# Performance work log

Measured on AMD Instinct MI355X. Metric: run time of the kernel, lower is better.

The kernel has to match this reference:

```python
import jax, jax.numpy as jnp
from jax import lax
import numpy as np

B_SZ, L, NH, DH, DS = 2, 2048, 24, 64, 128


def setup_inputs() -> dict:
    key = jax.random.key(0)
    k1, k2, k3, k4 = jax.random.split(key, 4)
    x = jax.random.normal(k1, (B_SZ, L, NH, DH), dtype=jnp.float32)
    A = jax.random.normal(k2, (B_SZ, L, NH), dtype=jnp.float32)
    B_mat = jax.random.normal(k3, (B_SZ, L, NH, DS), dtype=jnp.float32)
    C_mat = jax.random.normal(k4, (B_SZ, L, NH, DS), dtype=jnp.float32)
    delta_param = jnp.zeros((NH,), dtype=jnp.float32)
    return {"x": x, "A": A, "B_mat": B_mat, "C_mat": C_mat, "delta_param": delta_param}


def reference(x, A, B_mat, C_mat, delta_param):
    # x: (B, L, nh, dh); A: (B, L, nh); B_mat/C_mat: (B, L, nh, ds)
    b, l, nh, dh = x.shape
    ds = B_mat.shape[-1]
    delta = jax.nn.softplus(A + delta_param[None, None, :])        # (B, L, nh)
    A_bar = jnp.exp(-delta * jnp.abs(A))                            # (B, L, nh)

    def step(h, inp):
        x_t, B_t, C_t, a_t = inp  # (B,nh,dh), (B,nh,ds), (B,nh,ds), (B,nh)
        h = a_t[:, :, None, None] * h + x_t[..., None] * B_t[:, :, None, :]
        y_t = jnp.einsum('bhds,bhs->bhd', h, C_t)                   # (B, nh, dh)
        return h, y_t

    h0 = jnp.zeros((b, nh, dh, ds), dtype=x.dtype)
    xs = (jnp.moveaxis(x, 1, 0),      # (L, B, nh, dh)
          jnp.moveaxis(B_mat, 1, 0),  # (L, B, nh, ds)
          jnp.moveaxis(C_mat, 1, 0),  # (L, B, nh, ds)
          jnp.moveaxis(A_bar, 1, 0))  # (L, B, nh)
    _, ys = lax.scan(step, h0, xs)    # ys: (L, B, nh, dh)
    return jnp.moveaxis(ys, 0, 1)     # (B, L, nh, dh)
```

## Files before the change

kernel.cpp:

```cpp
#include <hip/hip_runtime.h>

#define B_SZ 2
#define LSEQ 2048
#define NHh 24
#define DHh 64
#define DSs 128
#define TCH 64
#define NC  (LSEQ / TCH)
#define BH  (B_SZ * NHh)

#define S_ELEMS   (BH * LSEQ)
#define G_ELEMS   ((size_t)BH * NC * DSs * DHh)
#define WS_S_BYTES ((size_t)S_ELEMS * 4)
#define WS_G_BYTES (G_ELEMS * 2)
#define WS_REQ     (WS_S_BYTES + 2 * WS_G_BYTES)

#define SP  136
#define UP  72

typedef __attribute__((ext_vector_type(8))) short bf16x8;
typedef __attribute__((ext_vector_type(4))) float f32x4;

__device__ __forceinline__ unsigned short f2bf(float f) {
    union { float f; unsigned u; } v; v.f = f;
    unsigned r = ((v.u >> 16) & 1u) + 0x7FFFu;
    return (unsigned short)((v.u + r) >> 16);
}
__device__ __forceinline__ float bf2f(unsigned short h) {
    union { unsigned u; float f; } v; v.u = ((unsigned)h) << 16; return v.f;
}
__device__ __forceinline__ unsigned pk2(float a, float b) {
    return (unsigned)f2bf(a) | ((unsigned)f2bf(b) << 16);
}

__global__ __launch_bounds__(256, 2)
void k1_chunk(const float* __restrict__ x, const float* __restrict__ A,
              const float* __restrict__ Bm, const float* __restrict__ dp,
              float* __restrict__ S_ws, unsigned short* __restrict__ G_ws) {
    __shared__ __align__(16) unsigned short sBT[DSs][UP];
    __shared__ __align__(16) unsigned short sXT[DHh][UP];
    __shared__ float sF[TCH];

    const int c  = blockIdx.x & (NC - 1);
    const int bh = blockIdx.x >> 5;
    const int nh = bh % NHh; const int b = bh / NHh;
    const int tid = threadIdx.x;
    const int lane = tid & 63;
    const int w = tid >> 6;

    const size_t row0 = (size_t)(b * LSEQ + c * TCH) * NHh + nh;

    const int u = tid >> 2;
    const int q = tid & 3;
    const float* Brow = Bm + (row0 + (size_t)u * NHh) * DSs;
    const float* xrow = x  + (row0 + (size_t)u * NHh) * DHh;
    float4 bv[8], xv[4];
    #pragma unroll
    for (int j = 0; j < 8; ++j) bv[j] = *(const float4*)(Brow + (j * 4 + q) * 4);
    #pragma unroll
    for (int j = 0; j < 4; ++j) xv[j] = *(const float4*)(xrow + (j * 4 + q) * 4);

    if (tid < 64) {
        float a  = A[row0 + (size_t)tid * NHh];
        float z  = a + dp[nh];
        float sp = (z > 20.0f) ? z : log1pf(expf(z));
        float la = -sp * fabsf(a);
        #pragma unroll
        for (int off = 1; off < 64; off <<= 1) {
            float v = __shfl_up(la, off, 64);
            if (lane >= off) la += v;
        }
        S_ws[(size_t)bh * LSEQ + c * TCH + tid] = la;
        float s63 = __shfl(la, 63, 64);
        sF[tid] = expf(s63 - la);
    }
    __syncthreads();

    #pragma unroll
    for (int j = 0; j < 8; ++j) {
        const int s = (j * 4 + q) * 4;
        sBT[s + 0][u] = f2bf(bv[j].x);
        sBT[s + 1][u] = f2bf(bv[j].y);
        sBT[s + 2][u] = f2bf(bv[j].z);
        sBT[s + 3][u] = f2bf(bv[j].w);
    }
    const float f = sF[u];
    #pragma unroll
    for (int j = 0; j < 4; ++j) {
        const int d = (j * 4 + q) * 4;
        sXT[d + 0][u] = f2bf(xv[j].x * f);
        sXT[d + 1][u] = f2bf(xv[j].y * f);
        sXT[d + 2][u] = f2bf(xv[j].z * f);
        sXT[d + 3][u] = f2bf(xv[j].w * f);
    }
    __syncthreads();

    const int fr = lane >> 4, fc = lane & 15;
    bf16x8 afr0 = *(const bf16x8*)&sXT[16 * w + fc][fr * 8];
    bf16x8 afr1 = *(const bf16x8*)&sXT[16 * w + fc][32 + fr * 8];
    #pragma unroll
    for (int st = 0; st < 8; ++st) {
        f32x4 acc = {0.f, 0.f, 0.f, 0.f};
        bf16x8 b0 = *(const bf16x8*)&sBT[st * 16 + fc][fr * 8];
        bf16x8 b1 = *(const bf16x8*)&sBT[st * 16 + fc][32 + fr * 8];
        acc = __builtin_amdgcn_mfma_f32_16x16x32_bf16(afr0, b0, acc, 0, 0, 0);
        acc = __builtin_amdgcn_mfma_f32_16x16x32_bf16(afr1, b1, acc, 0, 0, 0);
        unsigned short* gout = G_ws +
            ((((size_t)bh * NC + c) * DHh + 16 * w + fr * 4) * DSs) + st * 16 + fc;
        #pragma unroll
        for (int r = 0; r < 4; ++r) gout[(size_t)r * DSs] = f2bf(acc[r]);
    }
}

__global__ __launch_bounds__(256)
void k2_scan(const float* __restrict__ S_ws, const unsigned short* __restrict__ G_ws,
             unsigned short* __restrict__ H_ws) {
    const int dblk = blockIdx.x & 3;
    const int bh   = blockIdx.x >> 2;
    const int tid  = threadIdx.x;
    const int d    = dblk * 16 + (tid >> 4);
    const int s0   = (tid & 15) * 8;

    float h[8];
    #pragma unroll
    for (int k = 0; k < 8; ++k) h[k] = 0.f;

    size_t base = (((size_t)bh * NC) * DHh + d) * DSs + s0;
    const size_t cstride = (size_t)DHh * DSs;

    uint4 gv = *(const uint4*)(G_ws + base);
    for (int c = 0; c < NC; ++c) {
        uint4 gn = (c + 1 < NC) ? *(const uint4*)(G_ws + base + (size_t)(c + 1) * cstride) : gv;
        const float e = expf(S_ws[(size_t)bh * LSEQ + c * TCH + (TCH - 1)]);
        uint4 p;
        p.x = pk2(h[0], h[1]); p.y = pk2(h[2], h[3]);
        p.z = pk2(h[4], h[5]); p.w = pk2(h[6], h[7]);
        *(uint4*)(H_ws + base + (size_t)c * cstride) = p;
        const unsigned gu[4] = {gv.x, gv.y, gv.z, gv.w};
        #pragma unroll
        for (int k = 0; k < 4; ++k) {
            h[2 * k]     = fmaf(e, h[2 * k],     bf2f((unsigned short)(gu[k] & 0xffff)));
            h[2 * k + 1] = fmaf(e, h[2 * k + 1], bf2f((unsigned short)(gu[k] >> 16)));
        }
        gv = gn;
    }
}

__global__ __launch_bounds__(256, 2)
void k3_y(const float* __restrict__ x, const float* __restrict__ Bm,
          const float* __restrict__ Cm, const float* __restrict__ S_ws,
          const unsigned short* __restrict__ H_ws, float* __restrict__ y) {
    __shared__ __align__(16) unsigned short sC[TCH][SP];
    __shared__ __align__(16) unsigned short sB[TCH][SP];
    __shared__ __align__(16) unsigned short sH[DHh][SP];
    __shared__ __align__(16) unsigned short sW[TCH][UP];
    __shared__ __align__(16) unsigned short sXT[DHh][UP];
    __shared__ float sS[TCH];
    __shared__ float sEt[TCH];

    const int c  = blockIdx.x & (NC - 1);
    const int bh = blockIdx.x >> 5;
    const int nh = bh % NHh; const int b = bh / NHh;
    const int tid = threadIdx.x;
    const int lane = tid & 63;
    const int w = tid >> 6;

    const size_t row0 = (size_t)(b * LSEQ + c * TCH) * NHh + nh;

    const int rr = tid >> 2;
    const int q  = tid & 3;
    const float* Crow = Cm + (row0 + (size_t)rr * NHh) * DSs;
    const float* Brow = Bm + (row0 + (size_t)rr * NHh) * DSs;
    const float* xrow = x  + (row0 + (size_t)rr * NHh) * DHh;
    const unsigned short* Hrow = H_ws + (((size_t)bh * NC + c) * DHh + rr) * DSs;
    float4 cv[8], bv[8], xv[4];
    uint4  hv[4];
    #pragma unroll
    for (int j = 0; j < 8; ++j) cv[j] = *(const float4*)(Crow + (j * 4 + q) * 4);
    #pragma unroll
    for (int j = 0; j < 8; ++j) bv[j] = *(const float4*)(Brow + (j * 4 + q) * 4);
    #pragma unroll
    for (int j = 0; j < 4; ++j) xv[j] = *(const float4*)(xrow + (j * 4 + q) * 4);
    #pragma unroll
    for (int j = 0; j < 4; ++j) hv[j] = *(const uint4*)(Hrow + (j * 4 + q) * 8);

    if (tid < 64) {
        float sv = S_ws[(size_t)bh * LSEQ + c * TCH + tid];
        sS[tid]  = sv;
        sEt[tid] = expf(sv);
    }

    #pragma unroll
    for (int j = 0; j < 8; ++j) {
        const int s = (j * 4 + q) * 4;
        *(uint2*)&sC[rr][s] = make_uint2(pk2(cv[j].x, cv[j].y), pk2(cv[j].z, cv[j].w));
        *(uint2*)&sB[rr][s] = make_uint2(pk2(bv[j].x, bv[j].y), pk2(bv[j].z, bv[j].w));
    }
    #pragma unroll
    for (int j = 0; j < 4; ++j)
        *(uint4*)&sH[rr][(j * 4 + q) * 8] = hv[j];
    #pragma unroll
    for (int j = 0; j < 4; ++j) {
        const int d = (j * 4 + q) * 4;
        sXT[d + 0][rr] = f2bf(xv[j].x);
        sXT[d + 1][rr] = f2bf(xv[j].y);
        sXT[d + 2][rr] = f2bf(xv[j].z);
        sXT[d + 3][rr] = f2bf(xv[j].w);
    }
    __syncthreads();

    const int fr = lane >> 4, fc = lane & 15;
    const int t0w = 16 * w;

    bf16x8 ca[4];
    #pragma unroll
    for (int kb = 0; kb < 4; ++kb)
        ca[kb] = *(const bf16x8*)&sC[t0w + fc][kb * 32 + fr * 8];
    float st4[4];
    #pragma unroll
    for (int r = 0; r < 4; ++r) st4[r] = sS[t0w + fr * 4 + r];

    #pragma unroll
    for (int ut = 0; ut < 4; ++ut) {
        const int u0 = ut * 16;
        unsigned short wv[4] = {0, 0, 0, 0};
        if (ut <= w) {
            f32x4 acc = {0.f, 0.f, 0.f, 0.f};
            #pragma unroll
            for (int kb = 0; kb < 4; ++kb) {
                bf16x8 bb = *(const bf16x8*)&sB[u0 + fc][kb * 32 + fr * 8];
                acc = __builtin_amdgcn_mfma_f32_16x16x32_bf16(ca[kb], bb, acc, 0, 0, 0);
            }
            const float su = sS[u0 + fc];
            const int   uu = u0 + fc;
            #pragma unroll
            for (int r = 0; r < 4; ++r) {
                const int t = t0w + fr * 4 + r;
                const float dd = fminf(st4[r] - su, 0.f);
                const float val = (uu <= t) ? acc[r] * expf(dd) : 0.f;
                wv[r] = f2bf(val);
            }
        }
        #pragma unroll
        for (int r = 0; r < 4; ++r) sW[t0w + fr * 4 + r][u0 + fc] = wv[r];
    }

    bf16x8 wa0 = *(const bf16x8*)&sW[t0w + fc][fr * 8];
    bf16x8 wa1;
    if (w >= 2) wa1 = *(const bf16x8*)&sW[t0w + fc][32 + fr * 8];
    float et4[4];
    #pragma unroll
    for (int r = 0; r < 4; ++r) et4[r] = sEt[t0w + fr * 4 + r];

    #pragma unroll
    for (int dt = 0; dt < 4; ++dt) {
        const int d0 = dt * 16;
        f32x4 acc = {0.f, 0.f, 0.f, 0.f};
        #pragma unroll
        for (int kb = 0; kb < 4; ++kb) {
            bf16x8 hb = *(const bf16x8*)&sH[d0 + fc][kb * 32 + fr * 8];
            acc = __builtin_amdgcn_mfma_f32_16x16x32_bf16(ca[kb], hb, acc, 0, 0, 0);
        }
        #pragma unroll
        for (int r = 0; r < 4; ++r) acc[r] *= et4[r];
        bf16x8 xb0 = *(const bf16x8*)&sXT[d0 + fc][fr * 8];
        acc = __builtin_amdgcn_mfma_f32_16x16x32_bf16(wa0, xb0, acc, 0, 0, 0);
        if (w >= 2) {
            bf16x8 xb1 = *(const bf16x8*)&sXT[d0 + fc][32 + fr * 8];
            acc = __builtin_amdgcn_mfma_f32_16x16x32_bf16(wa1, xb1, acc, 0, 0, 0);
        }
        float* yout = y + (row0 + (size_t)(t0w + fr * 4) * NHh) * DHh + d0 + fc;
        #pragma unroll
        for (int r = 0; r < 4; ++r) yout[(size_t)r * NHh * DHh] = acc[r];
    }
}

__device__ __forceinline__ void gload_lds16(const float* g, void* l) {
    __builtin_amdgcn_global_load_lds(
        (const __attribute__((address_space(1))) void*)g,
        (__attribute__((address_space(3))) void*)l, 16, 0, 0);
}
__device__ __forceinline__ void gload_lds4(const float* g, float* l) {
    __builtin_amdgcn_global_load_lds(
        (const __attribute__((address_space(1))) void*)g,
        (__attribute__((address_space(3))) void*)l, 4, 0, 0);
}
#define F_DBLK 4
#define F_DPW 16
#define F_TCH 32
#define F_NCH (LSEQ / F_TCH)
__global__ __launch_bounds__(256, 1)
void ssm_scan_fb(const float* __restrict__ x, const float* __restrict__ A,
                 const float* __restrict__ Bm, const float* __restrict__ Cm,
                 const float* __restrict__ dp, float* __restrict__ y) {
    __shared__ float s_abar[LSEQ];
    __shared__ float s_B[2][F_TCH][DSs];
    __shared__ float s_C[2][F_TCH][DSs];
    __shared__ float s_x[2][F_TCH][F_DPW];
    const int blk = blockIdx.x;
    const int dblk = blk % F_DBLK, bh = blk / F_DBLK;
    const int nh = bh % NHh, b = bh / NHh;
    const float dpv = dp[nh];
    for (int i = threadIdx.x; i < LSEQ; i += 256) {
        float a = A[(b * LSEQ + i) * NHh + nh];
        float z = a + dpv;
        float sp = (z > 20.0f) ? z : log1pf(expf(z));
        s_abar[i] = expf(-sp * fabsf(a));
    }
    const int tid = threadIdx.x, wid = tid >> 6, lane = tid & 63;
    const int dloc = tid >> 4, sg = tid & 15, sb = sg * 8;
    const size_t bh_off = (size_t)(b * LSEQ) * NHh + nh;
    const float* Bbase = Bm + bh_off * DSs;
    const float* Cbase = Cm + bh_off * DSs;
    const float* xbase = x + bh_off * DHh + dblk * F_DPW;
    float* yp = y + bh_off * DHh + dblk * F_DPW + dloc;
    const int RSTRIDE = NHh * DSs, XSTRIDE = NHh * DHh;
    auto stage = [&](int buf, int t0) {
        #pragma unroll
        for (int j = 0; j < 4; ++j) {
            const int r0 = (wid * 4 + j) * 2, r = r0 + (lane >> 5), col = (lane & 31) * 4;
            gload_lds16(Bbase + (size_t)(t0 + r) * RSTRIDE + col, &s_B[buf][r0][0]);
            gload_lds16(Cbase + (size_t)(t0 + r) * RSTRIDE + col, &s_C[buf][r0][0]);
        }
        #pragma unroll
        for (int j = 0; j < 2; ++j) {
            const int idx = (wid * 2 + j) * 64 + lane, t = idx >> 4, dc = idx & 15;
            gload_lds4(xbase + (size_t)(t0 + t) * XSTRIDE + dc, &s_x[buf][(wid * 2 + j) * 4][0]);
        }
    };
    stage(0, 0);
    __syncthreads();
    float h0=0,h1=0,h2=0,h3=0,h4=0,h5=0,h6=0,h7=0;
    for (int c = 0; c < F_NCH; ++c) {
        const int buf = c & 1;
        if (c + 1 < F_NCH) stage(buf ^ 1, (c + 1) * F_TCH);
        const int t0 = c * F_TCH;
        #pragma unroll 4
        for (int tt = 0; tt < F_TCH; ++tt) {
            const int t = t0 + tt;
            const float a = s_abar[t], xd = s_x[buf][tt][dloc];
            const float4* Br = (const float4*)&s_B[buf][tt][sb];
            const float4* Cr = (const float4*)&s_C[buf][tt][sb];
            const float4 B0 = Br[0], B1 = Br[1], C0 = Cr[0], C1 = Cr[1];
            h0 = fmaf(a, h0, xd * B0.x); h1 = fmaf(a, h1, xd * B0.y);
            h2 = fmaf(a, h2, xd * B0.z); h3 = fmaf(a, h3, xd * B0.w);
            h4 = fmaf(a, h4, xd * B1.x); h5 = fmaf(a, h5, xd * B1.y);
            h6 = fmaf(a, h6, xd * B1.z); h7 = fmaf(a, h7, xd * B1.w);
            float p0 = h0 * C0.x; p0 = fmaf(h1, C0.y, p0); p0 = fmaf(h2, C0.z, p0); p0 = fmaf(h3, C0.w, p0);
            float p1 = h4 * C1.x; p1 = fmaf(h5, C1.y, p1); p1 = fmaf(h6, C1.z, p1); p1 = fmaf(h7, C1.w, p1);
            float p = p0 + p1;
            p += __shfl_xor(p, 1, 64); p += __shfl_xor(p, 2, 64);
            p += __shfl_xor(p, 4, 64); p += __shfl_xor(p, 8, 64);
            if (sg == 0) yp[(size_t)t * XSTRIDE] = p;
        }
        __syncthreads();
    }
}

extern "C" void kernel_launch(void* const* d_in, const int* in_sizes, int n_in,
                              void* d_out, int out_size, void* d_ws, size_t ws_size,
                              hipStream_t stream) {
    const float* x  = (const float*)d_in[0];
    const float* A  = (const float*)d_in[1];
    const float* Bm = (const float*)d_in[2];
    const float* Cm = (const float*)d_in[3];
    const float* dp = (const float*)d_in[4];
    float* y = (float*)d_out;

    if (ws_size >= WS_REQ) {
        float* S_ws = (float*)d_ws;
        unsigned short* G_ws = (unsigned short*)((char*)d_ws + WS_S_BYTES);
        unsigned short* H_ws = G_ws + G_ELEMS;
        hipLaunchKernelGGL(k1_chunk, dim3(BH * NC), dim3(256), 0, stream,
                           x, A, Bm, dp, S_ws, G_ws);
        hipLaunchKernelGGL(k2_scan, dim3(BH * 4), dim3(256), 0, stream,
                           S_ws, G_ws, H_ws);
        hipLaunchKernelGGL(k3_y, dim3(BH * NC), dim3(256), 0, stream,
                           x, Bm, Cm, S_ws, H_ws, y);
    } else {
        hipLaunchKernelGGL(ssm_scan_fb, dim3(BH * F_DBLK), dim3(256), 0, stream,
                           x, A, Bm, Cm, dp, y);
    }
}
```

Baseline: 188.9 us.

## Precompute bf16 swizzled B/C/x planes in k1 and DMA them into k3 LDS

k1 now also reads C and writes bf16 copies of B, C and raw x into workspace, laid out as XOR-swizzled planes. k3 then loads these planes straight into LDS with global_load_lds instead of loading fp32 rows and converting them through registers. k2 writes H in the same swizzled layout, caches the per-chunk decay exponentials in LDS and prefetches G two chunks ahead. This cuts k3's fp32 read traffic and conversion work but adds extra bf16 workspace writes in k1 and raises workspace size. If the workspace is too small, the fallback kernel runs instead.

```diff
diff --git a/kernel.cpp b/kernel.cpp
--- a/kernel.cpp
+++ b/kernel.cpp
@@ -9,14 +9,15 @@
 #define NC  (LSEQ / TCH)
 #define BH  (B_SZ * NHh)
 
-#define S_ELEMS   (BH * LSEQ)
-#define G_ELEMS   ((size_t)BH * NC * DSs * DHh)
-#define WS_S_BYTES ((size_t)S_ELEMS * 4)
-#define WS_G_BYTES (G_ELEMS * 2)
-#define WS_REQ     (WS_S_BYTES + 2 * WS_G_BYTES)
-
-#define SP  136
 #define UP  72
+
+#define S_ELEMS    ((size_t)BH * LSEQ)
+#define PLANE128   ((size_t)TCH * DSs)
+#define PLANE64    ((size_t)TCH * DHh)
+#define P128_ELEMS ((size_t)BH * NC * PLANE128)
+#define P64_ELEMS  ((size_t)BH * NC * PLANE64)
+#define WS_S_BYTES (S_ELEMS * 4)
+#define WS_REQ     (WS_S_BYTES + 4 * P128_ELEMS * 2 + P64_ELEMS * 2)
 
 typedef __attribute__((ext_vector_type(8))) short bf16x8;
 typedef __attribute__((ext_vector_type(4))) float f32x4;
@@ -32,13 +33,21 @@
 __device__ __forceinline__ unsigned pk2(float a, float b) {
     return (unsigned)f2bf(a) | ((unsigned)f2bf(b) << 16);
 }
+__device__ __forceinline__ void gload_lds16(const void* g, void* l) {
+    __builtin_amdgcn_global_load_lds(
+        (const __attribute__((address_space(1))) void*)g,
+        (__attribute__((address_space(3))) void*)l, 16, 0, 0);
+}
 
 __global__ __launch_bounds__(256, 2)
 void k1_chunk(const float* __restrict__ x, const float* __restrict__ A,
-              const float* __restrict__ Bm, const float* __restrict__ dp,
-              float* __restrict__ S_ws, unsigned short* __restrict__ G_ws) {
+              const float* __restrict__ Bm, const float* __restrict__ Cm,
+              const float* __restrict__ dp, float* __restrict__ S_ws,
+              unsigned short* __restrict__ G_ws, unsigned short* __restrict__ Bb_ws,
+              unsigned short* __restrict__ Cb_ws, unsigned short* __restrict__ Xb_ws) {
     __shared__ __align__(16) unsigned short sBT[DSs][UP];
-    __shared__ __align__(16) unsigned short sXT[DHh][UP];
+    __shared__ __align__(16) unsigned short sXTf[DHh][UP];
+    __shared__ __align__(16) unsigned short sXraw[DHh * DHh];
     __shared__ float sF[TCH];
 
     const int c  = blockIdx.x & (NC - 1);
@@ -53,10 +62,13 @@
     const int u = tid >> 2;
     const int q = tid & 3;
     const float* Brow = Bm + (row0 + (size_t)u * NHh) * DSs;
+    const float* Crow = Cm + (row0 + (size_t)u * NHh) * DSs;
     const float* xrow = x  + (row0 + (size_t)u * NHh) * DHh;
-    float4 bv[8], xv[4];
+    float4 bv[8], cv[8], xv[4];
     #pragma unroll
     for (int j = 0; j < 8; ++j) bv[j] = *(const float4*)(Brow + (j * 4 + q) * 4);
+    #pragma unroll
+    for (int j = 0; j < 8; ++j) cv[j] = *(const float4*)(Crow + (j * 4 + q) * 4);
     #pragma unroll
     for (int j = 0; j < 4; ++j) xv[j] = *(const float4*)(xrow + (j * 4 + q) * 4);
 
@@ -76,9 +88,17 @@
     }
     __syncthreads();
 
+    unsigned short* Bbo = Bb_ws + ((size_t)bh * NC + c) * PLANE128 + (size_t)u * DSs;
+    unsigned short* Cbo = Cb_ws + ((size_t)bh * NC + c) * PLANE128 + (size_t)u * DSs;
     #pragma unroll
     for (int j = 0; j < 8; ++j) {
-        const int s = (j * 4 + q) * 4;
+        const int sl   = j * 4 + q;
+        const int s    = sl * 4;
+        const int phys = ((sl >> 1) ^ (u & 7)) * 8 + (sl & 1) * 4;
+        uint2 bp; bp.x = pk2(bv[j].x, bv[j].y); bp.y = pk2(bv[j].z, bv[j].w);
+        uint2 cp; cp.x = pk2(cv[j].x, cv[j].y); cp.y = pk2(cv[j].z, cv[j].w);
+        *(uint2*)(Bbo + phys) = bp;
+        *(uint2*)(Cbo + phys) = cp;
         sBT[s + 0][u] = f2bf(bv[j].x);
         sBT[s + 1][u] = f2bf(bv[j].y);
         sBT[s + 2][u] = f2bf(bv[j].z);
@@ -87,17 +107,20 @@
     const float f = sF[u];
     #pragma unroll
     for (int j = 0; j < 4; ++j) {
-        const int d = (j * 4 + q) * 4;
-        sXT[d + 0][u] = f2bf(xv[j].x * f);
-        sXT[d + 1][u] = f2bf(xv[j].y * f);
-        sXT[d + 2][u] = f2bf(xv[j].z * f);
-        sXT[d + 3][u] = f2bf(xv[j].w * f);
+        const int d0 = (j * 4 + q) * 4;
+        const float xs[4] = {xv[j].x, xv[j].y, xv[j].z, xv[j].w};
+        #pragma unroll
+        for (int r = 0; r < 4; ++r) {
+            const int d = d0 + r;
+            sXTf[d][u] = f2bf(xs[r] * f);
+            sXraw[d * DHh + (((u >> 3) ^ (d & 7)) * 8) + (u & 7)] = f2bf(xs[r]);
+        }
     }
     __syncthreads();
 
     const int fr = lane >> 4, fc = lane & 15;
-    bf16x8 afr0 = *(const bf16x8*)&sXT[16 * w + fc][fr * 8];
-    bf16x8 afr1 = *(const bf16x8*)&sXT[16 * w + fc][32 + fr * 8];
+    bf16x8 afr0 = *(const bf16x8*)&sXTf[16 * w + fc][fr * 8];
+    bf16x8 afr1 = *(const bf16x8*)&sXTf[16 * w + fc][32 + fr * 8];
     #pragma unroll
     for (int st = 0; st < 8; ++st) {
         f32x4 acc = {0.f, 0.f, 0.f, 0.f};
@@ -106,55 +129,67 @@
         acc = __builtin_amdgcn_mfma_f32_16x16x32_bf16(afr0, b0, acc, 0, 0, 0);
         acc = __builtin_amdgcn_mfma_f32_16x16x32_bf16(afr1, b1, acc, 0, 0, 0);
         unsigned short* gout = G_ws +
-            ((((size_t)bh * NC + c) * DHh + 16 * w + fr * 4) * DSs) + st * 16 + fc;
+            (((size_t)bh * NC + c) * DHh + 16 * w + fr * 4) * DSs + st * 16 + fc;
         #pragma unroll
         for (int r = 0; r < 4; ++r) gout[(size_t)r * DSs] = f2bf(acc[r]);
     }
+
+    uint4* Xbo = (uint4*)(Xb_ws + ((size_t)bh * NC + c) * PLANE64);
+    const uint4* srcX = (const uint4*)sXraw;
+    #pragma unroll
+    for (int i = 0; i < 2; ++i) Xbo[i * 256 + tid] = srcX[i * 256 + tid];
 }
 
 __global__ __launch_bounds__(256)
 void k2_scan(const float* __restrict__ S_ws, const unsigned short* __restrict__ G_ws,
              unsigned short* __restrict__ H_ws) {
+    __shared__ float sE[NC];
     const int dblk = blockIdx.x & 3;
     const int bh   = blockIdx.x >> 2;
     const int tid  = threadIdx.x;
     const int d    = dblk * 16 + (tid >> 4);
     const int s0   = (tid & 15) * 8;
 
+    if (tid < NC) sE[tid] = expf(S_ws[(size_t)bh * LSEQ + tid * TCH + (TCH - 1)]);
+    __syncthreads();
+
+    const size_t cstride = PLANE128;
+    const size_t gbase = (size_t)bh * NC * PLANE128 + (size_t)d * DSs + s0;
+    const int    physs = ((s0 >> 3) ^ (d & 7)) * 8;
+    const size_t hbase = (size_t)bh * NC * PLANE128 + (size_t)d * DSs + physs;
+
     float h[8];
     #pragma unroll
     for (int k = 0; k < 8; ++k) h[k] = 0.f;
 
-    size_t base = (((size_t)bh * NC) * DHh + d) * DSs + s0;
-    const size_t cstride = (size_t)DHh * DSs;
-
-    uint4 gv = *(const uint4*)(G_ws + base);
+    uint4 g0 = *(const uint4*)(G_ws + gbase);
+    uint4 g1 = *(const uint4*)(G_ws + gbase + cstride);
     for (int c = 0; c < NC; ++c) {
-        uint4 gn = (c + 1 < NC) ? *(const uint4*)(G_ws + base + (size_t)(c + 1) * cstride) : gv;
-        const float e = expf(S_ws[(size_t)bh * LSEQ + c * TCH + (TCH - 1)]);
+        uint4 gn = (c + 2 < NC) ? *(const uint4*)(G_ws + gbase + (size_t)(c + 2) * cstride) : g0;
+        const float e = sE[c];
         uint4 p;
         p.x = pk2(h[0], h[1]); p.y = pk2(h[2], h[3]);
         p.z = pk2(h[4], h[5]); p.w = pk2(h[6], h[7]);
-        *(uint4*)(H_ws + base + (size_t)c * cstride) = p;
-        const unsigned gu[4] = {gv.x, gv.y, gv.z, gv.w};
+        *(uint4*)(H_ws + hbase + (size_t)c * cstride) = p;
+        const unsigned gu[4] = {g0.x, g0.y, g0.z, g0.w};
         #pragma unroll
         for (int k = 0; k < 4; ++k) {
             h[2 * k]     = fmaf(e, h[2 * k],     bf2f((unsigned short)(gu[k] & 0xffff)));
             h[2 * k + 1] = fmaf(e, h[2 * k + 1], bf2f((unsigned short)(gu[k] >> 16)));
         }
-        gv = gn;
+        g0 = g1; g1 = gn;
     }
 }
 
 __global__ __launch_bounds__(256, 2)
-void k3_y(const float* __restrict__ x, const float* __restrict__ Bm,
-          const float* __restrict__ Cm, const float* __restrict__ S_ws,
-          const unsigned short* __restrict__ H_ws, float* __restrict__ y) {
-    __shared__ __align__(16) unsigned short sC[TCH][SP];
-    __shared__ __align__(16) unsigned short sB[TCH][SP];
-    __shared__ __align__(16) unsigned short sH[DHh][SP];
+void k3_y(const unsigned short* __restrict__ Bb_ws, const unsigned short* __restrict__ Cb_ws,
+          const unsigned short* __restrict__ Xb_ws, const unsigned short* __restrict__ H_ws,
+          const float* __restrict__ S_ws, float* __restrict__ y) {
+    __shared__ __align__(16) unsigned short sC[TCH][DSs];
+    __shared__ __align__(16) unsigned short sB[TCH][DSs];
+    __shared__ __align__(16) unsigned short sH[DHh][DSs];
+    __shared__ __align__(16) unsigned short sXT[DHh][DHh];
     __shared__ __align__(16) unsigned short sW[TCH][UP];
-    __shared__ __align__(16) unsigned short sXT[DHh][UP];
     __shared__ float sS[TCH];
     __shared__ float sEt[TCH];
 
@@ -165,57 +200,36 @@
     const int lane = tid & 63;
     const int w = tid >> 6;
 
-    const size_t row0 = (size_t)(b * LSEQ + c * TCH) * NHh + nh;
-
-    const int rr = tid >> 2;
-    const int q  = tid & 3;
-    const float* Crow = Cm + (row0 + (size_t)rr * NHh) * DSs;
-    const float* Brow = Bm + (row0 + (size_t)rr * NHh) * DSs;
-    const float* xrow = x  + (row0 + (size_t)rr * NHh) * DHh;
-    const unsigned short* Hrow = H_ws + (((size_t)bh * NC + c) * DHh + rr) * DSs;
-    float4 cv[8], bv[8], xv[4];
-    uint4  hv[4];
-    #pragma unroll
-    for (int j = 0; j < 8; ++j) cv[j] = *(const float4*)(Crow + (j * 4 + q) * 4);
-    #pragma unroll
-    for (int j = 0; j < 8; ++j) bv[j] = *(const float4*)(Brow + (j * 4 + q) * 4);
-    #pragma unroll
-    for (int j = 0; j < 4; ++j) xv[j] = *(const float4*)(xrow + (j * 4 + q) * 4);
-    #pragma unroll
-    for (int j = 0; j < 4; ++j) hv[j] = *(const uint4*)(Hrow + (j * 4 + q) * 8);
-
+    const size_t p128 = ((size_t)bh * NC + c) * PLANE128;
+    const size_t p64  = ((size_t)bh * NC + c) * PLANE64;
+
+    #pragma unroll
+    for (int j = 0; j < 4; ++j) {
+        const int off = (w * 4 + j) * 512;
+        gload_lds16(Cb_ws + p128 + off + lane * 8, ((char*)&sC[0][0]) + off * 2);
+        gload_lds16(Bb_ws + p128 + off + lane * 8, ((char*)&sB[0][0]) + off * 2);
+        gload_lds16(H_ws  + p128 + off + lane * 8, ((char*)&sH[0][0]) + off * 2);
+    }
+    #pragma unroll
+    for (int j = 0; j < 2; ++j) {
+        const int off = (w * 2 + j) * 512;
+        gload_lds16(Xb_ws + p64 + off + lane * 8, ((char*)&sXT[0][0]) + off * 2);
+    }
     if (tid < 64) {
         float sv = S_ws[(size_t)bh * LSEQ + c * TCH + tid];
         sS[tid]  = sv;
         sEt[tid] = expf(sv);
     }
-
-    #pragma unroll
-    for (int j = 0; j < 8; ++j) {
-        const int s = (j * 4 + q) * 4;
-        *(uint2*)&sC[rr][s] = make_uint2(pk2(cv[j].x, cv[j].y), pk2(cv[j].z, cv[j].w));
-        *(uint2*)&sB[rr][s] = make_uint2(pk2(bv[j].x, bv[j].y), pk2(bv[j].z, bv[j].w));
-    }
-    #pragma unroll
-    for (int j = 0; j < 4; ++j)
-        *(uint4*)&sH[rr][(j * 4 + q) * 8] = hv[j];
-    #pragma unroll
-    for (int j = 0; j < 4; ++j) {
-        const int d = (j * 4 + q) * 4;
-        sXT[d + 0][rr] = f2bf(xv[j].x);
-        sXT[d + 1][rr] = f2bf(xv[j].y);
-        sXT[d + 2][rr] = f2bf(xv[j].z);
-        sXT[d + 3][rr] = f2bf(xv[j].w);
-    }
     __syncthreads();
 
     const int fr = lane >> 4, fc = lane & 15;
     const int t0w = 16 * w;
+    const int swz = fc & 7;
 
     bf16x8 ca[4];
     #pragma unroll
     for (int kb = 0; kb < 4; ++kb)
-        ca[kb] = *(const bf16x8*)&sC[t0w + fc][kb * 32 + fr * 8];
+        ca[kb] = *(const bf16x8*)&sC[t0w + fc][((kb * 4 + fr) ^ swz) * 8];
     float st4[4];
     #pragma unroll
     for (int r = 0; r < 4; ++r) st4[r] = sS[t0w + fr * 4 + r];
@@ -228,7 +242,7 @@
             f32x4 acc = {0.f, 0.f, 0.f, 0.f};
             #pragma unroll
             for (int kb = 0; kb < 4; ++kb) {
-                bf16x8 bb = *(const bf16x8*)&sB[u0 + fc][kb * 32 + fr * 8];
+                bf16x8 bb = *(const bf16x8*)&sB[u0 + fc][((kb * 4 + fr) ^ swz) * 8];
                 acc = __builtin_amdgcn_mfma_f32_16x16x32_bf16(ca[kb], bb, acc, 0, 0, 0);
             }
             const float su = sS[u0 + fc];
@@ -237,8 +251,7 @@
             for (int r = 0; r < 4; ++r) {
                 const int t = t0w + fr * 4 + r;
                 const float dd = fminf(st4[r] - su, 0.f);
-                const float val = (uu <= t) ? acc[r] * expf(dd) : 0.f;
-                wv[r] = f2bf(val);
+                wv[r] = f2bf((uu <= t) ? acc[r] * expf(dd) : 0.f);
             }
         }
         #pragma unroll
@@ -252,21 +265,22 @@
     #pragma unroll
     for (int r = 0; r < 4; ++r) et4[r] = sEt[t0w + fr * 4 + r];
 
+    const size_t row0 = (size_t)(b * LSEQ + c * TCH) * NHh + nh;
     #pragma unroll
     for (int dt = 0; dt < 4; ++dt) {
         const int d0 = dt * 16;
         f32x4 acc = {0.f, 0.f, 0.f, 0.f};
         #pragma unroll
         for (int kb = 0; kb < 4; ++kb) {
-            bf16x8 hb = *(const bf16x8*)&sH[d0 + fc][kb * 32 + fr * 8];
+            bf16x8 hb = *(const bf16x8*)&sH[d0 + fc][((kb * 4 + fr) ^ swz) * 8];
             acc = __builtin_amdgcn_mfma_f32_16x16x32_bf16(ca[kb], hb, acc, 0, 0, 0);
         }
         #pragma unroll
         for (int r = 0; r < 4; ++r) acc[r] *= et4[r];
-        bf16x8 xb0 = *(const bf16x8*)&sXT[d0 + fc][fr * 8];
+        bf16x8 xb0 = *(const bf16x8*)&sXT[d0 + fc][((0 + fr) ^ swz) * 8];
         acc = __builtin_amdgcn_mfma_f32_16x16x32_bf16(wa0, xb0, acc, 0, 0, 0);
         if (w >= 2) {
-            bf16x8 xb1 = *(const bf16x8*)&sXT[d0 + fc][32 + fr * 8];
+            bf16x8 xb1 = *(const bf16x8*)&sXT[d0 + fc][((4 + fr) ^ swz) * 8];
             acc = __builtin_amdgcn_mfma_f32_16x16x32_bf16(wa1, xb1, acc, 0, 0, 0);
         }
         float* yout = y + (row0 + (size_t)(t0w + fr * 4) * NHh) * DHh + d0 + fc;
@@ -275,11 +289,6 @@
     }
 }
 
-__device__ __forceinline__ void gload_lds16(const float* g, void* l) {
-    __builtin_amdgcn_global_load_lds(
-        (const __attribute__((address_space(1))) void*)g,
-        (__attribute__((address_space(3))) void*)l, 16, 0, 0);
-}
 __device__ __forceinline__ void gload_lds4(const float* g, float* l) {
     __builtin_amdgcn_global_load_lds(
         (const __attribute__((address_space(1))) void*)g,
@@ -369,14 +378,17 @@
 
     if (ws_size >= WS_REQ) {
         float* S_ws = (float*)d_ws;
-        unsigned short* G_ws = (unsigned short*)((char*)d_ws + WS_S_BYTES);
-        unsigned short* H_ws = G_ws + G_ELEMS;
+        unsigned short* G_ws  = (unsigned short*)((char*)d_ws + WS_S_BYTES);
+        unsigned short* H_ws  = G_ws + P128_ELEMS;
+        unsigned short* Bb_ws = H_ws + P128_ELEMS;
+        unsigned short* Cb_ws = Bb_ws + P128_ELEMS;
+        unsigned short* Xb_ws = Cb_ws + P128_ELEMS;
         hipLaunchKernelGGL(k1_chunk, dim3(BH * NC), dim3(256), 0, stream,
-                           x, A, Bm, dp, S_ws, G_ws);
+                           x, A, Bm, Cm, dp, S_ws, G_ws, Bb_ws, Cb_ws, Xb_ws);
         hipLaunchKernelGGL(k2_scan, dim3(BH * 4), dim3(256), 0, stream,
                            S_ws, G_ws, H_ws);
         hipLaunchKernelGGL(k3_y, dim3(BH * NC), dim3(256), 0, stream,
-                           x, Bm, Cm, S_ws, H_ws, y);
+                           Bb_ws, Cb_ws, Xb_ws, H_ws, S_ws, y);
     } else {
         hipLaunchKernelGGL(ssm_scan_fb, dim3(BH * F_DBLK), dim3(256), 0, stream,
                            x, A, Bm, Cm, dp, y);
```

Result: slower. 209.0 us (+10.6%).

## Stage chunk states through LDS and split inter-chunk scan across more blocks

Applied to the files above, without the earlier changes.

k1 now writes its per-chunk G tile into shared memory and then stores it with coalesced 16-byte writes, instead of scattered 2-byte global stores. k2 runs as 768 blocks of 64 threads rather than 192 blocks of 256, so more of the GPU is busy on the serial chunk scan. k2 also precomputes the per-chunk decay factors into shared memory and prefetches two chunks ahead to hide load latency. The cost is extra LDS in k1, which may lower occupancy, and smaller blocks in k2.

```diff
diff --git a/kernel.cpp b/kernel.cpp
--- a/kernel.cpp
+++ b/kernel.cpp
@@ -9,14 +9,15 @@
 #define NC  (LSEQ / TCH)
 #define BH  (B_SZ * NHh)
 
-#define S_ELEMS   (BH * LSEQ)
-#define G_ELEMS   ((size_t)BH * NC * DSs * DHh)
-#define WS_S_BYTES ((size_t)S_ELEMS * 4)
-#define WS_G_BYTES (G_ELEMS * 2)
-#define WS_REQ     (WS_S_BYTES + 2 * WS_G_BYTES)
-
 #define SP  136
 #define UP  72
+#define GP  144
+
+#define S_ELEMS    ((size_t)BH * LSEQ)
+#define PLANE128   ((size_t)TCH * DSs)
+#define P128_ELEMS ((size_t)BH * NC * PLANE128)
+#define WS_S_BYTES (S_ELEMS * 4)
+#define WS_REQ     (WS_S_BYTES + 2 * P128_ELEMS * 2)
 
 typedef __attribute__((ext_vector_type(8))) short bf16x8;
 typedef __attribute__((ext_vector_type(4))) float f32x4;
@@ -31,6 +32,11 @@
 }
 __device__ __forceinline__ unsigned pk2(float a, float b) {
     return (unsigned)f2bf(a) | ((unsigned)f2bf(b) << 16);
+}
+__device__ __forceinline__ void gload_lds16(const void* g, void* l) {
+    __builtin_amdgcn_global_load_lds(
+        (const __attribute__((address_space(1))) void*)g,
+        (__attribute__((address_space(3))) void*)l, 16, 0, 0);
 }
 
 __global__ __launch_bounds__(256, 2)
@@ -38,7 +44,8 @@
               const float* __restrict__ Bm, const float* __restrict__ dp,
               float* __restrict__ S_ws, unsigned short* __restrict__ G_ws) {
     __shared__ __align__(16) unsigned short sBT[DSs][UP];
-    __shared__ __align__(16) unsigned short sXT[DHh][UP];
+    __shared__ __align__(16) unsigned short sXTf[DHh][UP];
+    __shared__ __align__(16) unsigned short sG[DHh][GP];
     __shared__ float sF[TCH];
 
     const int c  = blockIdx.x & (NC - 1);
@@ -88,16 +95,16 @@
     #pragma unroll
     for (int j = 0; j < 4; ++j) {
         const int d = (j * 4 + q) * 4;
-        sXT[d + 0][u] = f2bf(xv[j].x * f);
-        sXT[d + 1][u] = f2bf(xv[j].y * f);
-        sXT[d + 2][u] = f2bf(xv[j].z * f);
-        sXT[d + 3][u] = f2bf(xv[j].w * f);
+        sXTf[d + 0][u] = f2bf(xv[j].x * f);
+        sXTf[d + 1][u] = f2bf(xv[j].y * f);
+        sXTf[d + 2][u] = f2bf(xv[j].z * f);
+        sXTf[d + 3][u] = f2bf(xv[j].w * f);
     }
     __syncthreads();
 
     const int fr = lane >> 4, fc = lane & 15;
-    bf16x8 afr0 = *(const bf16x8*)&sXT[16 * w + fc][fr * 8];
-    bf16x8 afr1 = *(const bf16x8*)&sXT[16 * w + fc][32 + fr * 8];
+    bf16x8 afr0 = *(const bf16x8*)&sXTf[16 * w + fc][fr * 8];
+    bf16x8 afr1 = *(const bf16x8*)&sXTf[16 * w + fc][32 + fr * 8];
     #pragma unroll
     for (int st = 0; st < 8; ++st) {
         f32x4 acc = {0.f, 0.f, 0.f, 0.f};
@@ -105,44 +112,58 @@
         bf16x8 b1 = *(const bf16x8*)&sBT[st * 16 + fc][32 + fr * 8];
         acc = __builtin_amdgcn_mfma_f32_16x16x32_bf16(afr0, b0, acc, 0, 0, 0);
         acc = __builtin_amdgcn_mfma_f32_16x16x32_bf16(afr1, b1, acc, 0, 0, 0);
-        unsigned short* gout = G_ws +
-            ((((size_t)bh * NC + c) * DHh + 16 * w + fr * 4) * DSs) + st * 16 + fc;
-        #pragma unroll
-        for (int r = 0; r < 4; ++r) gout[(size_t)r * DSs] = f2bf(acc[r]);
-    }
-}
-
-__global__ __launch_bounds__(256)
+        #pragma unroll
+        for (int r = 0; r < 4; ++r)
+            sG[16 * w + fr * 4 + r][st * 16 + fc] = f2bf(acc[r]);
+    }
+    __syncthreads();
+
+    const size_t gplane = ((size_t)bh * NC + c) * PLANE128;
+    #pragma unroll
+    for (int i = 0; i < 4; ++i) {
+        const int idx = i * 256 + tid;
+        const int row = idx >> 4;
+        const int col = (idx & 15) * 8;
+        *(uint4*)(G_ws + gplane + (size_t)row * DSs + col) = *(const uint4*)&sG[row][col];
+    }
+}
+
+__global__ __launch_bounds__(64)
 void k2_scan(const float* __restrict__ S_ws, const unsigned short* __restrict__ G_ws,
              unsigned short* __restrict__ H_ws) {
-    const int dblk = blockIdx.x & 3;
-    const int bh   = blockIdx.x >> 2;
+    __shared__ float sE[NC];
+    const int dblk = blockIdx.x & 15;
+    const int bh   = blockIdx.x >> 4;
     const int tid  = threadIdx.x;
-    const int d    = dblk * 16 + (tid >> 4);
+    const int d    = dblk * 4 + (tid >> 4);
     const int s0   = (tid & 15) * 8;
 
+    if (tid < NC) sE[tid] = expf(S_ws[(size_t)bh * LSEQ + tid * TCH + (TCH - 1)]);
+    __syncthreads();
+
+    const size_t cstride = PLANE128;
+    const size_t base = (size_t)bh * NC * PLANE128 + (size_t)d * DSs + s0;
+
     float h[8];
     #pragma unroll
     for (int k = 0; k < 8; ++k) h[k] = 0.f;
 
-    size_t base = (((size_t)bh * NC) * DHh + d) * DSs + s0;
-    const size_t cstride = (size_t)DHh * DSs;
-
-    uint4 gv = *(const uint4*)(G_ws + base);
+    uint4 g0 = *(const uint4*)(G_ws + base);
+    uint4 g1 = *(const uint4*)(G_ws + base + cstride);
     for (int c = 0; c < NC; ++c) {
-        uint4 gn = (c + 1 < NC) ? *(const uint4*)(G_ws + base + (size_t)(c + 1) * cstride) : gv;
-        const float e = expf(S_ws[(size_t)bh * LSEQ + c * TCH + (TCH - 1)]);
+        uint4 gn = (c + 2 < NC) ? *(const uint4*)(G_ws + base + (size_t)(c + 2) * cstride) : g0;
+        const float e = sE[c];
         uint4 p;
         p.x = pk2(h[0], h[1]); p.y = pk2(h[2], h[3]);
         p.z = pk2(h[4], h[5]); p.w = pk2(h[6], h[7]);
         *(uint4*)(H_ws + base + (size_t)c * cstride) = p;
-        const unsigned gu[4] = {gv.x, gv.y, gv.z, gv.w};
+        const unsigned gu[4] = {g0.x, g0.y, g0.z, g0.w};
         #pragma unroll
         for (int k = 0; k < 4; ++k) {
             h[2 * k]     = fmaf(e, h[2 * k],     bf2f((unsigned short)(gu[k] & 0xffff)));
             h[2 * k + 1] = fmaf(e, h[2 * k + 1], bf2f((unsigned short)(gu[k] >> 16)));
         }
-        gv = gn;
+        g0 = g1; g1 = gn;
     }
 }
 
@@ -237,8 +258,7 @@
             for (int r = 0; r < 4; ++r) {
                 const int t = t0w + fr * 4 + r;
                 const float dd = fminf(st4[r] - su, 0.f);
-                const float val = (uu <= t) ? acc[r] * expf(dd) : 0.f;
-                wv[r] = f2bf(val);
+                wv[r] = f2bf((uu <= t) ? acc[r] * expf(dd) : 0.f);
             }
         }
         #pragma unroll
@@ -275,11 +295,6 @@
     }
 }
 
-__device__ __forceinline__ void gload_lds16(const float* g, void* l) {
-    __builtin_amdgcn_global_load_lds(
-        (const __attribute__((address_space(1))) void*)g,
-        (__attribute__((address_space(3))) void*)l, 16, 0, 0);
-}
 __device__ __forceinline__ void gload_lds4(const float* g, float* l) {
     __builtin_amdgcn_global_load_lds(
         (const __attribute__((address_space(1))) void*)g,
@@ -370,10 +385,10 @@
     if (ws_size >= WS_REQ) {
         float* S_ws = (float*)d_ws;
         unsigned short* G_ws = (unsigned short*)((char*)d_ws + WS_S_BYTES);
-        unsigned short* H_ws = G_ws + G_ELEMS;
+        unsigned short* H_ws = G_ws + P128_ELEMS;
         hipLaunchKernelGGL(k1_chunk, dim3(BH * NC), dim3(256), 0, stream,
                            x, A, Bm, dp, S_ws, G_ws);
-        hipLaunchKernelGGL(k2_scan, dim3(BH * 4), dim3(256), 0, stream,
+        hipLaunchKernelGGL(k2_scan, dim3(BH * 16), dim3(64), 0, stream,
                            S_ws, G_ws, H_ws);
         hipLaunchKernelGGL(k3_y, dim3(BH * NC), dim3(256), 0, stream,
                            x, Bm, Cm, S_ws, H_ws, y);
```

Result: no change. 190.0 us (+0.6%).
